# Performance work log

Hardware: AMD Instinct MI355X
Metric: run time of the kernel (lower is better)

## Reference

```python
import jax, jax.numpy as jnp
import numpy as np

SEQ_LEN = 12          # seq_length
K = 8                 # nsamples = 2 * num_samples
RADII = (4.0 + 1e-06, 8.0 + 1e-06, 12.0 + 1e-06)
COUT = (64, 128, 256)


def _group(xyz, s_xyz, radius):
    # ball query via knn + radius mask: xyz (B,N,3) queries, s_xyz (B,M,3) keys
    d2 = jnp.sum((xyz[:, :, None, :] - s_xyz[:, None, :, :]) ** 2, axis=-1)  # (B,N,M)
    neg, idx = jax.lax.top_k(-d2, K)                                          # (B,N,K)
    valid = (-neg) <= radius * radius
    # points outside the ball are replaced by the nearest neighbor (pad-with-first)
    return jnp.where(valid, idx, idx[..., :1])


def _gather(a, idx):
    # a (B,M,C), idx (B,N,K) -> (B,N,K,C)
    return jax.vmap(lambda t, i: t[i])(a, idx)


def _cell(xyz, feat, state, W, b, radius, cout):
    # PointRNN cell: group state points around current points, fuse
    # [displacement, current feature, state feature] with a shared linear,
    # then max-pool over the K neighbors. New state xyz = current xyz.
    B, N, _ = xyz.shape
    if state is None:
        s_xyz, s_feat = xyz, jnp.zeros((B, N, cout), xyz.dtype)
    else:
        s_xyz, s_feat = state
    idx = _group(xyz, s_xyz, radius)
    n_xyz = _gather(s_xyz, idx)                      # (B,N,K,3)
    n_feat = _gather(s_feat, idx)                    # (B,N,K,cout)
    disp = n_xyz - xyz[:, :, None, :]
    parts = [disp]
    if feat is not None:
        cin = feat.shape[-1]
        parts.append(jnp.broadcast_to(feat[:, :, None, :], (B, N, K, cin)))
    parts.append(n_feat)
    h = jnp.concatenate(parts, axis=-1) @ W + b      # (B,N,K,cout)
    return (xyz, jnp.max(h, axis=2))                 # (xyz, (B,N,cout))


def _forward(frames, W1, b1, W2, b2, W3, b3, Wm, bm, Wl, bl):
    half = SEQ_LEN // 2
    s1 = s2 = s3 = None
    # encode
    for i in range(half):
        s1 = _cell(frames[:, i], None, s1, W1, b1, RADII[0], COUT[0])
        s2 = _cell(s1[0], s1[1], s2, W2, b2, RADII[1], COUT[1])
        s3 = _cell(s2[0], s2[1], s3, W3, b3, RADII[2], COUT[2])
    # decode
    input_frame = frames[:, half - 1]
    preds = []
    for i in range(half, SEQ_LEN):
        s1 = _cell(input_frame, None, s1, W1, b1, RADII[0], COUT[0])
        s2 = _cell(s1[0], s1[1], s2, W2, b2, RADII[1], COUT[1])
        s3 = _cell(s2[0], s2[1], s3, W3, b3, RADII[2], COUT[2])
        h = jax.nn.relu(s3[1] @ Wm + bm)             # MLP([256,64]) = Lin+ReLU
        motion = h @ Wl + bl                         # (B,N,3)
        input_frame = input_frame + motion
        preds.append(input_frame)
    return jnp.stack(preds, axis=1)                  # (B, T/2, N, 3)


def setup_inputs() -> dict:
    key = jax.random.key(0)
    ks = jax.random.split(key, 12)
    B, N = 16, 512
    frames = jax.random.normal(ks[0], (B, SEQ_LEN, N, 3), jnp.float32) * 2.0

    def lin(k, fin, fout):
        k1, k2 = jax.random.split(k)
        s = 1.0 / np.sqrt(fin)
        return (jax.random.uniform(k1, (fin, fout), jnp.float32, -s, s),
                jax.random.uniform(k2, (fout,), jnp.float32, -s, s))

    W1, b1 = lin(ks[1], 3 + 0 + 64, 64)
    W2, b2 = lin(ks[2], 3 + 64 + 128, 128)
    W3, b3 = lin(ks[3], 3 + 128 + 256, 256)
    Wm, bm = lin(ks[4], 256, 64)
    Wl, bl = lin(ks[5], 64, 3)
    return {"frames": frames, "W1": W1, "b1": b1, "W2": W2, "b2": b2,
            "W3": W3, "b3": b3, "Wm": Wm, "bm": bm, "Wl": Wl, "bl": bl}


def reference(frames, W1, b1, W2, b2, W3, b3, Wm, bm, Wl, bl):
    return _forward(frames, W1, b1, W2, b2, W3, b3, Wm, bm, Wl, bl)
```

## Files before the change

### kernel.cpp

```cpp
#include <hip/hip_runtime.h>
#include <math.h>

#define BB 16
#define NN 512
#define KNN 8
#define SEQ 12
#define TQ 8
#define QB 32
#define PB 16

typedef __attribute__((ext_vector_type(8))) short bf8_t;
typedef __attribute__((ext_vector_type(4))) float f4_t;

__device__ __forceinline__ ushort f2b(float x) {
    uint u = __float_as_uint(x);
    return (ushort)((u + 0x7fffu + ((u >> 16) & 1u)) >> 16);
}
__device__ __forceinline__ float b2f(ushort h) {
    return __uint_as_float((uint)h << 16);
}
__device__ __forceinline__ void cvt8(const float* __restrict__ p,
                                     bf8_t& h, bf8_t& l) {
    float4 x0 = *(const float4*)p;
    float4 x1 = *(const float4*)(p + 4);
    float v[8] = {x0.x, x0.y, x0.z, x0.w, x1.x, x1.y, x1.z, x1.w};
#pragma unroll
    for (int i = 0; i < 8; ++i) {
        ushort hh = f2b(v[i]);
        h[i] = (short)hh;
        l[i] = (short)f2b(v[i] - b2f(hh));
    }
}

__global__ __launch_bounds__(256) void knn_kernel(
        const float* __restrict__ xq, int xq_bs,
        const float* __restrict__ xs, int xs_bs,
        int* __restrict__ idx1, int* __restrict__ idx2, int* __restrict__ idx3,
        float r2a, float r2b, float r2c, int warm) {
    __shared__ float s[NN * 3 + NN / 64];
    __shared__ float cd[QB][TQ][KNN + 1];
    __shared__ int   ci[QB][TQ][KNN + 1];
    int b = blockIdx.y;
    const float* xqp; const float* xsp; long iofs;
    if (warm) {
        int z = blockIdx.z;
        int qz = z < 5 ? z : 5;
        int sz = z - 1 < 0 ? 0 : z - 1;
        xqp = xq + (long)qz * NN * 3;
        xsp = xq + (long)sz * NN * 3;
        xs_bs = xq_bs;
        iofs = (long)z * BB * NN * KNN;
    } else {
        xqp = xq; xsp = xs; iofs = 0;
    }

    for (int j = threadIdx.x; j < NN; j += 256) {
        const float* p = xsp + (long)b * xs_bs + j * 3;
        int o = 3 * j + (j >> 6);
        s[o + 0] = p[0]; s[o + 1] = p[1]; s[o + 2] = p[2];
    }
    __syncthreads();

    int qi  = threadIdx.x / TQ;
    int sub = threadIdx.x % TQ;
    int n = blockIdx.x * QB + qi;
    const float* q = xqp + (long)b * xq_bs + n * 3;
    float qx = q[0], qy = q[1], qz2 = q[2];

    float bd[KNN];
    int   bi[KNN];
#pragma unroll
    for (int k = 0; k < KNN; ++k) { bd[k] = 1e30f; bi[k] = 0; }

    int j0 = sub * (NN / TQ);
    int sbase = 3 * j0 + sub;
#pragma unroll 4
    for (int jj = 0; jj < NN / TQ; ++jj) {
        float dx = s[sbase + 3 * jj + 0] - qx;
        float dy = s[sbase + 3 * jj + 1] - qy;
        float dz = s[sbase + 3 * jj + 2] - qz2;
        float d2 = fmaf(dx, dx, fmaf(dy, dy, dz * dz));
        if (d2 < bd[KNN - 1]) {
            bd[KNN - 1] = d2; bi[KNN - 1] = j0 + jj;
#pragma unroll
            for (int k = KNN - 1; k >= 1; --k) {
                if (bd[k] < bd[k - 1]) {
                    float td = bd[k]; bd[k] = bd[k - 1]; bd[k - 1] = td;
                    int   ti = bi[k]; bi[k] = bi[k - 1]; bi[k - 1] = ti;
                }
            }
        }
    }

#pragma unroll
    for (int k = 0; k < KNN; ++k) { cd[qi][sub][k] = bd[k]; ci[qi][sub][k] = bi[k]; }
    cd[qi][sub][KNN] = 1e30f; ci[qi][sub][KNN] = 0x7fffffff;
    __syncthreads();

    for (int stride = TQ / 2; stride >= 1; stride >>= 1) {
        if (sub < stride) {
            float rd[KNN]; int ri[KNN];
            int ia = 0, ib = 0;
#pragma unroll
            for (int k = 0; k < KNN; ++k) {
                float da = cd[qi][sub][ia], db = cd[qi][sub + stride][ib];
                int   ja = ci[qi][sub][ia], jb = ci[qi][sub + stride][ib];
                bool ta = (da < db) || (da == db && ja < jb);
                rd[k] = ta ? da : db; ri[k] = ta ? ja : jb;
                ia += ta ? 1 : 0; ib += ta ? 0 : 1;
            }
#pragma unroll
            for (int k = 0; k < KNN; ++k) { cd[qi][sub][k] = rd[k]; ci[qi][sub][k] = ri[k]; }
        }
        __syncthreads();
    }

    if (sub == 0) {
        long base = iofs + ((long)(b * NN + n)) * KNN;
        int i0 = ci[qi][0][0];
#pragma unroll
        for (int k = 0; k < KNN; ++k) {
            float d = cd[qi][0][k]; int j = ci[qi][0][k];
            idx1[base + k] = (d <= r2a) ? j : i0;
            idx2[base + k] = (d <= r2b) ? j : i0;
            idx3[base + k] = (d <= r2c) ? j : i0;
        }
    }
}

__global__ __launch_bounds__(256) void convW_kernel(
        const float* __restrict__ W1, const float* __restrict__ W2,
        const float* __restrict__ W3, const float* __restrict__ Wm,
        ushort* __restrict__ w1h, ushort* __restrict__ w1l,
        ushort* __restrict__ w2h, ushort* __restrict__ w2l,
        ushort* __restrict__ w3h, ushort* __restrict__ w3l,
        ushort* __restrict__ w2fh, ushort* __restrict__ w2fl,
        ushort* __restrict__ w3fh, ushort* __restrict__ w3fl,
        ushort* __restrict__ wmh, ushort* __restrict__ wml) {
    int t = blockIdx.x * 256 + threadIdx.x;
    float v; ushort* ph; ushort* pl; int idx;
    if (t < 4096)        { int n = t >> 6, k = t & 63;
        v = W1[(3 + k) * 64 + n];   ph = w1h;  pl = w1l;  idx = t; }
    else if (t < 20480)  { int u = t - 4096, n = u >> 7, k = u & 127;
        v = W2[(67 + k) * 128 + n]; ph = w2h;  pl = w2l;  idx = u; }
    else if (t < 86016)  { int u = t - 20480, n = u >> 8, k = u & 255;
        v = W3[(131 + k) * 256 + n]; ph = w3h; pl = w3l;  idx = u; }
    else if (t < 94208)  { int u = t - 86016, n = u >> 6, k = u & 63;
        v = W2[(3 + k) * 128 + n];  ph = w2fh; pl = w2fl; idx = u; }
    else if (t < 126976) { int u = t - 94208, n = u >> 7, k = u & 127;
        v = W3[(3 + k) * 256 + n];  ph = w3fh; pl = w3fl; idx = u; }
    else if (t < 143360) { int u = t - 126976, n = u >> 8, k = u & 255;
        v = Wm[k * 64 + n];         ph = wmh;  pl = wml;  idx = u; }
    else return;
    ushort h = f2b(v);
    ph[idx] = h; pl[idx] = f2b(v - b2f(h));
}

template<bool FIRST>
__global__ __launch_bounds__(512, 4) void cells_kernel(
        const float* __restrict__ xq, int xq_bs,
        const float* __restrict__ xs, int xs_bs,
        const int* __restrict__ i1, const int* __restrict__ i2,
        const int* __restrict__ i3,
        const float* __restrict__ G1p, const float* __restrict__ G2p,
        const float* __restrict__ G3p,
        ushort* __restrict__ s1h, ushort* __restrict__ s1l,
        ushort* __restrict__ s2h, ushort* __restrict__ s2l,
        ushort* __restrict__ s3h, ushort* __restrict__ s3l,
        const float* __restrict__ W1, const float* __restrict__ b1,
        const float* __restrict__ W2, const float* __restrict__ b2,
        const float* __restrict__ W3, const float* __restrict__ b3,
        const ushort* __restrict__ w2fh, const ushort* __restrict__ w2fl,
        const ushort* __restrict__ w3fh, const ushort* __restrict__ w3fl,
        const ushort* __restrict__ wmh, const ushort* __restrict__ wml,
        const float* __restrict__ bm,
        const float* __restrict__ Wl, const float* __restrict__ bl,
        float* __restrict__ xnext, int xn_bs, int do_head) {
    __shared__ float s1s[PB][68];
    __shared__ float s2s[PB][132];
    __shared__ float s3b[PB][260];
    __shared__ float hs[PB][64];
    __shared__ float dsp[3][PB][KNN][3];
    __shared__ int   jss[3][PB][KNN];

    const int tid = threadIdx.x;
    const int blk = blockIdx.x;
    const int xcd = blk & 7, slot = blk >> 3;
    const int b   = xcd * 2 + (slot >> 5);
    const int n0  = (slot & 31) << 4;
    const long row0 = (long)b * NN + n0;
    const long bN = (long)b * NN;
    const int wv = tid >> 6, lane = tid & 63;
    const int fm = lane & 15, quad = lane >> 4;

    for (int t = tid; t < 3 * PB * KNN; t += 512) {
        int r = t >> 7, rem = t & 127, p = rem >> 3, k = rem & 7;
        const int* ix = (r == 0) ? i1 : ((r == 1) ? i2 : i3);
        int j = ix[(row0 + p) * KNN + k];
        jss[r][p][k] = j;
        const float* sp = xs + (long)b * xs_bs + j * 3;
        const float* qp = xq + (long)b * xq_bs + (n0 + p) * 3;
        dsp[r][p][k][0] = sp[0] - qp[0];
        dsp[r][p][k][1] = sp[1] - qp[1];
        dsp[r][p][k][2] = sp[2] - qp[2];
    }
    __syncthreads();

    {
        int co = tid & 63, q = tid >> 6;
        float g1r[2][KNN];
        if (!FIRST) {
#pragma unroll
            for (int r = 0; r < 2; ++r)
#pragma unroll
                for (int k = 0; k < KNN; ++k)
                    g1r[r][k] = G1p[(bN + jss[0][2 * q + r][k]) * 64 + co];
        }
        float wx = W1[co], wy = W1[64 + co], wz = W1[128 + co];
        float bz = b1[co];
#pragma unroll
        for (int r = 0; r < 2; ++r) {
            int p = 2 * q + r;
            float acc = -1e30f;
#pragma unroll
            for (int k = 0; k < KNN; ++k) {
                float v = fmaf(dsp[0][p][k][0], wx, bz);
                v = fmaf(dsp[0][p][k][1], wy, v);
                v = fmaf(dsp[0][p][k][2], wz, v);
                if (!FIRST) v += g1r[r][k];
                acc = fmaxf(acc, v);
            }
            s1s[p][co] = acc;
            ushort h = f2b(acc);
            s1h[(row0 + p) * 64 + co] = h;
            s1l[(row0 + p) * 64 + co] = f2b(acc - b2f(h));
        }
    }
    __syncthreads();

    float4 g2r[KNN];
    {
        int c4 = tid & 31, g = tid >> 5;
        if (!FIRST) {
#pragma unroll
            for (int k = 0; k < KNN; ++k)
                g2r[k] = ((const float4*)G2p)[(bN + jss[1][g][k]) * 32 + c4];
        }
    }

    {
        int col = wv * 16 + fm;
        float bz = b2[col];
        f4_t acc = {bz, bz, bz, bz};
#pragma unroll
        for (int k0 = 0; k0 < 64; k0 += 32) {
            bf8_t ah, al; cvt8(&s1s[fm][k0 + quad * 8], ah, al);
            bf8_t bh = *(const bf8_t*)(w2fh + col * 64 + k0 + quad * 8);
            bf8_t bl = *(const bf8_t*)(w2fl + col * 64 + k0 + quad * 8);
            acc = __builtin_amdgcn_mfma_f32_16x16x32_bf16(ah, bh, acc, 0, 0, 0);
            acc = __builtin_amdgcn_mfma_f32_16x16x32_bf16(ah, bl, acc, 0, 0, 0);
            acc = __builtin_amdgcn_mfma_f32_16x16x32_bf16(al, bh, acc, 0, 0, 0);
        }
#pragma unroll
        for (int r = 0; r < 4; ++r) s2s[quad * 4 + r][col] = acc[r];
    }
    __syncthreads();

    {
        int c4 = tid & 31, g = tid >> 5;
        float4 bse = *(float4*)&s2s[g][c4 * 4];
        float4 wx = ((const float4*)W2)[c4];
        float4 wy = ((const float4*)(W2 + 128))[c4];
        float4 wz = ((const float4*)(W2 + 256))[c4];
        float4 m = make_float4(-1e30f, -1e30f, -1e30f, -1e30f);
#pragma unroll
        for (int k = 0; k < KNN; ++k) {
            float dx = dsp[1][g][k][0], dy = dsp[1][g][k][1], dz = dsp[1][g][k][2];
            float4 v;
            v.x = fmaf(dz, wz.x, fmaf(dy, wy.x, fmaf(dx, wx.x, bse.x)));
            v.y = fmaf(dz, wz.y, fmaf(dy, wy.y, fmaf(dx, wx.y, bse.y)));
            v.z = fmaf(dz, wz.z, fmaf(dy, wy.z, fmaf(dx, wx.z, bse.z)));
            v.w = fmaf(dz, wz.w, fmaf(dy, wy.w, fmaf(dx, wx.w, bse.w)));
            if (!FIRST) {
                v.x += g2r[k].x; v.y += g2r[k].y;
                v.z += g2r[k].z; v.w += g2r[k].w;
            }
            m.x = fmaxf(m.x, v.x); m.y = fmaxf(m.y, v.y);
            m.z = fmaxf(m.z, v.z); m.w = fmaxf(m.w, v.w);
        }
        *(float4*)&s2s[g][c4 * 4] = m;
        ushort4 mh, ml;
        mh.x = f2b(m.x); ml.x = f2b(m.x - b2f(mh.x));
        mh.y = f2b(m.y); ml.y = f2b(m.y - b2f(mh.y));
        mh.z = f2b(m.z); ml.z = f2b(m.z - b2f(mh.z));
        mh.w = f2b(m.w); ml.w = f2b(m.w - b2f(mh.w));
        *(ushort4*)&s2h[(row0 + g) * 128 + c4 * 4] = mh;
        *(ushort4*)&s2l[(row0 + g) * 128 + c4 * 4] = ml;
    }
    __syncthreads();

    float4 g3r[2][KNN];
    {
        int c4 = tid & 63, g = tid >> 6;
        if (!FIRST) {
#pragma unroll
            for (int r = 0; r < 2; ++r)
#pragma unroll
                for (int k = 0; k < KNN; ++k)
                    g3r[r][k] = ((const float4*)G3p)[(bN + jss[2][2 * g + r][k]) * 64 + c4];
        }
    }

    {
        int col0 = wv * 16 + fm, col1 = (wv + 8) * 16 + fm;
        float bz0 = b3[col0], bz1 = b3[col1];
        f4_t a0 = {bz0, bz0, bz0, bz0};
        f4_t a1 = {bz1, bz1, bz1, bz1};
#pragma unroll
        for (int k0 = 0; k0 < 128; k0 += 32) {
            bf8_t ah, al; cvt8(&s2s[fm][k0 + quad * 8], ah, al);
            bf8_t b0h = *(const bf8_t*)(w3fh + col0 * 128 + k0 + quad * 8);
            bf8_t b0l = *(const bf8_t*)(w3fl + col0 * 128 + k0 + quad * 8);
            bf8_t b1h = *(const bf8_t*)(w3fh + col1 * 128 + k0 + quad * 8);
            bf8_t b1l = *(const bf8_t*)(w3fl + col1 * 128 + k0 + quad * 8);
            a0 = __builtin_amdgcn_mfma_f32_16x16x32_bf16(ah, b0h, a0, 0, 0, 0);
            a0 = __builtin_amdgcn_mfma_f32_16x16x32_bf16(ah, b0l, a0, 0, 0, 0);
            a0 = __builtin_amdgcn_mfma_f32_16x16x32_bf16(al, b0h, a0, 0, 0, 0);
            a1 = __builtin_amdgcn_mfma_f32_16x16x32_bf16(ah, b1h, a1, 0, 0, 0);
            a1 = __builtin_amdgcn_mfma_f32_16x16x32_bf16(ah, b1l, a1, 0, 0, 0);
            a1 = __builtin_amdgcn_mfma_f32_16x16x32_bf16(al, b1h, a1, 0, 0, 0);
        }
#pragma unroll
        for (int r = 0; r < 4; ++r) {
            s3b[quad * 4 + r][col0] = a0[r];
            s3b[quad * 4 + r][col1] = a1[r];
        }
    }
    __syncthreads();

    {
        int c4 = tid & 63, g = tid >> 6;
        float4 wx = ((const float4*)W3)[c4];
        float4 wy = ((const float4*)(W3 + 256))[c4];
        float4 wz = ((const float4*)(W3 + 512))[c4];
#pragma unroll
        for (int r = 0; r < 2; ++r) {
            int p = 2 * g + r;
            float4 bse = *(float4*)&s3b[p][c4 * 4];
            float4 m = make_float4(-1e30f, -1e30f, -1e30f, -1e30f);
#pragma unroll
            for (int k = 0; k < KNN; ++k) {
                float dx = dsp[2][p][k][0], dy = dsp[2][p][k][1], dz = dsp[2][p][k][2];
                float4 v;
                v.x = fmaf(dz, wz.x, fmaf(dy, wy.x, fmaf(dx, wx.x, bse.x)));
                v.y = fmaf(dz, wz.y, fmaf(dy, wy.y, fmaf(dx, wx.y, bse.y)));
                v.z = fmaf(dz, wz.z, fmaf(dy, wy.z, fmaf(dx, wx.z, bse.z)));
                v.w = fmaf(dz, wz.w, fmaf(dy, wy.w, fmaf(dx, wx.w, bse.w)));
                if (!FIRST) {
                    v.x += g3r[r][k].x; v.y += g3r[r][k].y;
                    v.z += g3r[r][k].z; v.w += g3r[r][k].w;
                }
                m.x = fmaxf(m.x, v.x); m.y = fmaxf(m.y, v.y);
                m.z = fmaxf(m.z, v.z); m.w = fmaxf(m.w, v.w);
            }
            *(float4*)&s3b[p][c4 * 4] = m;
            ushort4 mh, ml;
            mh.x = f2b(m.x); ml.x = f2b(m.x - b2f(mh.x));
            mh.y = f2b(m.y); ml.y = f2b(m.y - b2f(mh.y));
            mh.z = f2b(m.z); ml.z = f2b(m.z - b2f(mh.z));
            mh.w = f2b(m.w); ml.w = f2b(m.w - b2f(mh.w));
            *(ushort4*)&s3h[(row0 + p) * 256 + c4 * 4] = mh;
            *(ushort4*)&s3l[(row0 + p) * 256 + c4 * 4] = ml;
        }
    }

    if (do_head) {
        __syncthreads();
        if (wv < 4) {
            int col = wv * 16 + fm;
            float bz = bm[col];
            f4_t acc = {bz, bz, bz, bz};
#pragma unroll
            for (int k0 = 0; k0 < 256; k0 += 32) {
                bf8_t ah, al; cvt8(&s3b[fm][k0 + quad * 8], ah, al);
                bf8_t bh = *(const bf8_t*)(wmh + col * 256 + k0 + quad * 8);
                bf8_t bl = *(const bf8_t*)(wml + col * 256 + k0 + quad * 8);
                acc = __builtin_amdgcn_mfma_f32_16x16x32_bf16(ah, bh, acc, 0, 0, 0);
                acc = __builtin_amdgcn_mfma_f32_16x16x32_bf16(ah, bl, acc, 0, 0, 0);
                acc = __builtin_amdgcn_mfma_f32_16x16x32_bf16(al, bh, acc, 0, 0, 0);
            }
#pragma unroll
            for (int r = 0; r < 4; ++r)
                hs[quad * 4 + r][col] = fmaxf(acc[r], 0.f);
        }
        __syncthreads();
        if (tid < PB * 3) {
            int p = tid / 3, d = tid % 3;
            float m = bl[d];
#pragma unroll 4
            for (int c = 0; c < 64; ++c)
                m = fmaf(hs[p][c], Wl[c * 3 + d], m);
            const float* qp = xq + (long)b * xq_bs + (n0 + p) * 3;
            xnext[(long)b * xn_bs + (n0 + p) * 3 + d] = qp[d] + m;
        }
    }
}

template<int N>
__device__ __forceinline__ void gemmTile(
        const ushort* __restrict__ Ah, const ushort* __restrict__ Al,
        const ushort* __restrict__ Bh, const ushort* __restrict__ Bl,
        float* __restrict__ G, int rb, int cb, int tid, ushort* lds) {
    const int row0 = rb * 128, c0 = cb * 64;
    ushort* ah = lds;
    ushort* al = lds + 128 * 40;
    ushort* bh = lds + 256 * 40;
    ushort* bl = lds + 320 * 40;
    const int wv = tid >> 6, lane = tid & 63;
    const int m = lane & 15, quad = lane >> 4;
    const int wm0 = wv * 32;
    const int lr = tid >> 2, ls = (tid & 3) * 8;

    f4_t acc[2][4];
#pragma unroll
    for (int rt = 0; rt < 2; ++rt)
#pragma unroll
        for (int ct = 0; ct < 4; ++ct) acc[rt][ct] = (f4_t){0.f, 0.f, 0.f, 0.f};

    bf8_t pah0, pah1, pal0, pal1, pbh, pbl;
    pah0 = *(const bf8_t*)(Ah + (long)(row0 + lr) * N + ls);
    pah1 = *(const bf8_t*)(Ah + (long)(row0 + 64 + lr) * N + ls);
    pal0 = *(const bf8_t*)(Al + (long)(row0 + lr) * N + ls);
    pal1 = *(const bf8_t*)(Al + (long)(row0 + 64 + lr) * N + ls);
    pbh  = *(const bf8_t*)(Bh + (long)(c0 + lr) * N + ls);
    pbl  = *(const bf8_t*)(Bl + (long)(c0 + lr) * N + ls);

    for (int k0 = 0; k0 < N; k0 += 32) {
        if (k0) __syncthreads();
        *(bf8_t*)(ah + lr * 40 + ls) = pah0;
        *(bf8_t*)(ah + (64 + lr) * 40 + ls) = pah1;
        *(bf8_t*)(al + lr * 40 + ls) = pal0;
        *(bf8_t*)(al + (64 + lr) * 40 + ls) = pal1;
        *(bf8_t*)(bh + lr * 40 + ls) = pbh;
        *(bf8_t*)(bl + lr * 40 + ls) = pbl;
        __syncthreads();
        if (k0 + 32 < N) {
            int kn = k0 + 32;
            pah0 = *(const bf8_t*)(Ah + (long)(row0 + lr) * N + kn + ls);
            pah1 = *(const bf8_t*)(Ah + (long)(row0 + 64 + lr) * N + kn + ls);
            pal0 = *(const bf8_t*)(Al + (long)(row0 + lr) * N + kn + ls);
            pal1 = *(const bf8_t*)(Al + (long)(row0 + 64 + lr) * N + kn + ls);
            pbh  = *(const bf8_t*)(Bh + (long)(c0 + lr) * N + kn + ls);
            pbl  = *(const bf8_t*)(Bl + (long)(c0 + lr) * N + kn + ls);
        }
        bf8_t a0h = *(const bf8_t*)(ah + (wm0 + m) * 40 + quad * 8);
        bf8_t a0l = *(const bf8_t*)(al + (wm0 + m) * 40 + quad * 8);
        bf8_t a1h = *(const bf8_t*)(ah + (wm0 + 16 + m) * 40 + quad * 8);
        bf8_t a1l = *(const bf8_t*)(al + (wm0 + 16 + m) * 40 + quad * 8);
#pragma unroll
        for (int ct = 0; ct < 4; ++ct) {
            bf8_t bth = *(const bf8_t*)(bh + (ct * 16 + m) * 40 + quad * 8);
            bf8_t btl = *(const bf8_t*)(bl + (ct * 16 + m) * 40 + quad * 8);
            acc[0][ct] = __builtin_amdgcn_mfma_f32_16x16x32_bf16(a0h, bth, acc[0][ct], 0, 0, 0);
            acc[0][ct] = __builtin_amdgcn_mfma_f32_16x16x32_bf16(a0h, btl, acc[0][ct], 0, 0, 0);
            acc[0][ct] = __builtin_amdgcn_mfma_f32_16x16x32_bf16(a0l, bth, acc[0][ct], 0, 0, 0);
            acc[1][ct] = __builtin_amdgcn_mfma_f32_16x16x32_bf16(a1h, bth, acc[1][ct], 0, 0, 0);
            acc[1][ct] = __builtin_amdgcn_mfma_f32_16x16x32_bf16(a1h, btl, acc[1][ct], 0, 0, 0);
            acc[1][ct] = __builtin_amdgcn_mfma_f32_16x16x32_bf16(a1l, bth, acc[1][ct], 0, 0, 0);
        }
    }
#pragma unroll
    for (int rt = 0; rt < 2; ++rt)
#pragma unroll
        for (int ct = 0; ct < 4; ++ct) {
            int col = c0 + ct * 16 + m;
#pragma unroll
            for (int r = 0; r < 4; ++r)
                G[(long)(row0 + wm0 + rt * 16 + quad * 4 + r) * N + col] = acc[rt][ct][r];
        }
}

__global__ __launch_bounds__(256) void gemmG_kernel(
        const ushort* __restrict__ s1h, const ushort* __restrict__ s1l,
        const ushort* __restrict__ s2h, const ushort* __restrict__ s2l,
        const ushort* __restrict__ s3h, const ushort* __restrict__ s3l,
        const ushort* __restrict__ w1h, const ushort* __restrict__ w1l,
        const ushort* __restrict__ w2h, const ushort* __restrict__ w2l,
        const ushort* __restrict__ w3h, const ushort* __restrict__ w3l,
        float* __restrict__ G1, float* __restrict__ G2,
        float* __restrict__ G3) {
    __shared__ ushort lds[384 * 40];
    int bx = blockIdx.x, tid = threadIdx.x;
    if (bx < 256) {
        int xcd = bx & 7, rem = bx >> 3;
        int rb = xcd * 8 + (rem & 7), cb = rem >> 3;
        gemmTile<256>(s3h, s3l, w3h, w3l, G3, rb, cb, tid, lds);
    } else if (bx < 384) {
        int u = bx - 256; int xcd = u & 7, rem = u >> 3;
        int rb = xcd * 8 + (rem & 7), cb = rem >> 3;
        gemmTile<128>(s2h, s2l, w2h, w2l, G2, rb, cb, tid, lds);
    } else {
        int u = bx - 384; int xcd = u & 7, j = u >> 3;
        gemmTile<64>(s1h, s1l, w1h, w1l, G1, xcd * 8 + j, 0, tid, lds);
    }
}

extern "C" void kernel_launch(void* const* d_in, const int* in_sizes, int n_in,
                              void* d_out, int out_size, void* d_ws, size_t ws_size,
                              hipStream_t stream) {
    const float* frames = (const float*)d_in[0];
    const float* W1 = (const float*)d_in[1]; const float* b1 = (const float*)d_in[2];
    const float* W2 = (const float*)d_in[3]; const float* b2 = (const float*)d_in[4];
    const float* W3 = (const float*)d_in[5]; const float* b3 = (const float*)d_in[6];
    const float* Wm = (const float*)d_in[7]; const float* bm = (const float*)d_in[8];
    const float* Wl = (const float*)d_in[9]; const float* bl = (const float*)d_in[10];
    float* out = (float*)d_out;

    const long M = (long)BB * NN;
    float* ws = (float*)d_ws;
    float* G1b = ws; ws += M * 64;
    float* G2b = ws; ws += M * 128;
    float* G3b = ws; ws += M * 256;
    ushort* us = (ushort*)ws;
    ushort* s1h = us; us += M * 64;   ushort* s1l = us; us += M * 64;
    ushort* s2h = us; us += M * 128;  ushort* s2l = us; us += M * 128;
    ushort* s3h = us; us += M * 256;  ushort* s3l = us; us += M * 256;
    ushort* w1h = us; us += 4096;     ushort* w1l = us; us += 4096;
    ushort* w2h = us; us += 16384;    ushort* w2l = us; us += 16384;
    ushort* w3h = us; us += 65536;    ushort* w3l = us; us += 65536;
    ushort* w2fh = us; us += 8192;    ushort* w2fl = us; us += 8192;
    ushort* w3fh = us; us += 32768;   ushort* w3fl = us; us += 32768;
    ushort* wmh = us; us += 16384;    ushort* wml = us; us += 16384;
    const long BNK = M * KNN;
    int* ip = (int*)us;
    int* idx1w = ip; ip += 7 * BNK;
    int* idx2w = ip; ip += 7 * BNK;
    int* idx3w = ip; ip += 7 * BNK;

    double ra = 4.0 + 1e-6, rb = 8.0 + 1e-6, rc = 12.0 + 1e-6;
    float r2a = (float)(ra * ra), r2b = (float)(rb * rb), r2c = (float)(rc * rc);

    const int FB = SEQ * NN * 3;
    const int OB = 6 * NN * 3;

    convW_kernel<<<560, 256, 0, stream>>>(W1, W2, W3, Wm,
                                          w1h, w1l, w2h, w2l, w3h, w3l,
                                          w2fh, w2fl, w3fh, w3fl, wmh, wml);
    knn_kernel<<<dim3(NN / QB, BB, 7), 256, 0, stream>>>(
        frames, FB, nullptr, 0, idx1w, idx2w, idx3w, r2a, r2b, r2c, 1);

    for (int t = 0; t < SEQ; ++t) {
        const float* xq; int xq_bs;
        const float* xs; int xs_bs;
        if (t < 6)       { xq = frames + (long)t * NN * 3;        xq_bs = FB; }
        else if (t == 6) { xq = frames + 5L * NN * 3;             xq_bs = FB; }
        else             { xq = out + (long)(t - 7) * NN * 3;     xq_bs = OB; }
        if (t == 0)      { xs = xq;                               xs_bs = xq_bs; }
        else if (t <= 6) { xs = frames + (long)(t - 1) * NN * 3;  xs_bs = FB; }
        else if (t == 7) { xs = frames + 5L * NN * 3;             xs_bs = FB; }
        else             { xs = out + (long)(t - 8) * NN * 3;     xs_bs = OB; }

        int slot = (t <= 6) ? t : 0;
        int* i1 = idx1w + slot * BNK;
        int* i2 = idx2w + slot * BNK;
        int* i3 = idx3w + slot * BNK;

        if (t >= 7)
            knn_kernel<<<dim3(NN / QB, BB, 1), 256, 0, stream>>>(
                xq, xq_bs, xs, xs_bs, i1, i2, i3, r2a, r2b, r2c, 0);

        int do_head = (t >= 6);
        float* xnext = do_head ? out + (long)(t - 6) * NN * 3 : nullptr;

        if (t == 0)
            cells_kernel<true><<<BB * NN / PB, 512, 0, stream>>>(
                xq, xq_bs, xs, xs_bs, i1, i2, i3,
                G1b, G2b, G3b, s1h, s1l, s2h, s2l, s3h, s3l,
                W1, b1, W2, b2, W3, b3,
                w2fh, w2fl, w3fh, w3fl, wmh, wml, bm,
                Wl, bl, xnext, OB, do_head);
        else
            cells_kernel<false><<<BB * NN / PB, 512, 0, stream>>>(
                xq, xq_bs, xs, xs_bs, i1, i2, i3,
                G1b, G2b, G3b, s1h, s1l, s2h, s2l, s3h, s3l,
                W1, b1, W2, b2, W3, b3,
                w2fh, w2fl, w3fh, w3fl, wmh, wml, bm,
                Wl, bl, xnext, OB, do_head);

        if (t < SEQ - 1)
            gemmG_kernel<<<448, 256, 0, stream>>>(
                s1h, s1l, s2h, s2l, s3h, s3l,
                w1h, w1l, w2h, w2l, w3h, w3l,
                G1b, G2b, G3b);
    }
}
```

Before: 555.6 us.

## Fuse decode KNN into gemmG launch and store bf16 hi/lo splits in LDS

Decode-step KNN for the next timestep is now computed by extra blocks appended to the G-matrix GEMM launch, removing a separate kernel launch and letting KNN overlap the GEMM. The cells kernel stores hi/lo bf16 splits of intermediate states directly in a pooled, aliased LDS buffer instead of fp32 arrays that were re-converted before each MFMA. This trades repeated conversion work for extra LDS stores and more careful shared-memory aliasing.

```diff
diff --git a/kernel.cpp b/kernel.cpp
--- a/kernel.cpp
+++ b/kernel.cpp
@@ -18,18 +18,6 @@
 }
 __device__ __forceinline__ float b2f(ushort h) {
     return __uint_as_float((uint)h << 16);
-}
-__device__ __forceinline__ void cvt8(const float* __restrict__ p,
-                                     bf8_t& h, bf8_t& l) {
-    float4 x0 = *(const float4*)p;
-    float4 x1 = *(const float4*)(p + 4);
-    float v[8] = {x0.x, x0.y, x0.z, x0.w, x1.x, x1.y, x1.z, x1.w};
-#pragma unroll
-    for (int i = 0; i < 8; ++i) {
-        ushort hh = f2b(v[i]);
-        h[i] = (short)hh;
-        l[i] = (short)f2b(v[i] - b2f(hh));
-    }
 }
 
 __global__ __launch_bounds__(256) void knn_kernel(
@@ -121,6 +109,91 @@
 #pragma unroll
         for (int k = 0; k < KNN; ++k) {
             float d = cd[qi][0][k]; int j = ci[qi][0][k];
+            idx1[base + k] = (d <= r2a) ? j : i0;
+            idx2[base + k] = (d <= r2b) ? j : i0;
+            idx3[base + k] = (d <= r2c) ? j : i0;
+        }
+    }
+}
+
+__device__ void knn_core(const float* __restrict__ xq, int xq_bs,
+                         const float* __restrict__ xs, int xs_bs,
+                         int* __restrict__ idx1, int* __restrict__ idx2,
+                         int* __restrict__ idx3,
+                         float r2a, float r2b, float r2c,
+                         int bx, int b, int tid, char* smem) {
+    float* s  = (float*)smem;
+    float* cd = s + 1544;
+    int*   ci = (int*)(cd + 2304);
+
+    for (int j = tid; j < NN; j += 256) {
+        const float* p = xs + (long)b * xs_bs + j * 3;
+        int o = 3 * j + (j >> 6);
+        s[o + 0] = p[0]; s[o + 1] = p[1]; s[o + 2] = p[2];
+    }
+    __syncthreads();
+
+    int qi = tid / TQ, sub = tid % TQ;
+    int n = bx * QB + qi;
+    const float* q = xq + (long)b * xq_bs + n * 3;
+    float qx = q[0], qy = q[1], qz2 = q[2];
+
+    float bd[KNN]; int bi[KNN];
+#pragma unroll
+    for (int k = 0; k < KNN; ++k) { bd[k] = 1e30f; bi[k] = 0; }
+
+    int j0 = sub * (NN / TQ);
+    int sbase = 3 * j0 + sub;
+#pragma unroll 4
+    for (int jj = 0; jj < NN / TQ; ++jj) {
+        float dx = s[sbase + 3 * jj + 0] - qx;
+        float dy = s[sbase + 3 * jj + 1] - qy;
+        float dz = s[sbase + 3 * jj + 2] - qz2;
+        float d2 = fmaf(dx, dx, fmaf(dy, dy, dz * dz));
+        if (d2 < bd[KNN - 1]) {
+            bd[KNN - 1] = d2; bi[KNN - 1] = j0 + jj;
+#pragma unroll
+            for (int k = KNN - 1; k >= 1; --k) {
+                if (bd[k] < bd[k - 1]) {
+                    float td = bd[k]; bd[k] = bd[k - 1]; bd[k - 1] = td;
+                    int   ti = bi[k]; bi[k] = bi[k - 1]; bi[k - 1] = ti;
+                }
+            }
+        }
+    }
+
+    int b9 = (qi * 8 + sub) * 9;
+#pragma unroll
+    for (int k = 0; k < KNN; ++k) { cd[b9 + k] = bd[k]; ci[b9 + k] = bi[k]; }
+    cd[b9 + KNN] = 1e30f; ci[b9 + KNN] = 0x7fffffff;
+    __syncthreads();
+
+    for (int stride = TQ / 2; stride >= 1; stride >>= 1) {
+        if (sub < stride) {
+            int a9 = (qi * 8 + sub) * 9, c9 = (qi * 8 + sub + stride) * 9;
+            float rd[KNN]; int ri[KNN];
+            int ia = 0, ib = 0;
+#pragma unroll
+            for (int k = 0; k < KNN; ++k) {
+                float da = cd[a9 + ia], db = cd[c9 + ib];
+                int   ja = ci[a9 + ia], jb = ci[c9 + ib];
+                bool ta = (da < db) || (da == db && ja < jb);
+                rd[k] = ta ? da : db; ri[k] = ta ? ja : jb;
+                ia += ta ? 1 : 0; ib += ta ? 0 : 1;
+            }
+#pragma unroll
+            for (int k = 0; k < KNN; ++k) { cd[a9 + k] = rd[k]; ci[a9 + k] = ri[k]; }
+        }
+        __syncthreads();
+    }
+
+    if (sub == 0) {
+        int a9 = (qi * 8) * 9;
+        long base = ((long)(b * NN + n)) * KNN;
+        int i0 = ci[a9];
+#pragma unroll
+        for (int k = 0; k < KNN; ++k) {
+            float d = cd[a9 + k]; int j = ci[a9 + k];
             idx1[base + k] = (d <= r2a) ? j : i0;
             idx2[base + k] = (d <= r2b) ? j : i0;
             idx3[base + k] = (d <= r2c) ? j : i0;
@@ -176,12 +249,18 @@
         const float* __restrict__ bm,
         const float* __restrict__ Wl, const float* __restrict__ bl,
         float* __restrict__ xnext, int xn_bs, int do_head) {
-    __shared__ float s1s[PB][68];
-    __shared__ float s2s[PB][132];
-    __shared__ float s3b[PB][260];
-    __shared__ float hs[PB][64];
-    __shared__ float dsp[3][PB][KNN][3];
-    __shared__ int   jss[3][PB][KNN];
+    __shared__ __attribute__((aligned(16))) char pool[44544];
+    float*  dspf = (float*)pool;
+    int*    jssp = (int*)(pool + 4608);
+    ushort* s1H  = (ushort*)(pool + 6144);
+    ushort* s1L  = (ushort*)(pool + 8448);
+    float*  s2sp = (float*)(pool + 10752);
+    ushort* s2H  = (ushort*)(pool + 19200);
+    ushort* s2L  = (ushort*)(pool + 23552);
+    float*  s3bp = (float*)(pool + 27904);
+    ushort* s3H  = (ushort*)(pool + 6144);
+    ushort* s3L  = (ushort*)(pool + 14592);
+    float*  hsp  = (float*)pool;
 
     const int tid = threadIdx.x;
     const int blk = blockIdx.x;
@@ -197,12 +276,12 @@
         int r = t >> 7, rem = t & 127, p = rem >> 3, k = rem & 7;
         const int* ix = (r == 0) ? i1 : ((r == 1) ? i2 : i3);
         int j = ix[(row0 + p) * KNN + k];
-        jss[r][p][k] = j;
+        jssp[t] = j;
         const float* sp = xs + (long)b * xs_bs + j * 3;
         const float* qp = xq + (long)b * xq_bs + (n0 + p) * 3;
-        dsp[r][p][k][0] = sp[0] - qp[0];
-        dsp[r][p][k][1] = sp[1] - qp[1];
-        dsp[r][p][k][2] = sp[2] - qp[2];
+        dspf[t * 3 + 0] = sp[0] - qp[0];
+        dspf[t * 3 + 1] = sp[1] - qp[1];
+        dspf[t * 3 + 2] = sp[2] - qp[2];
     }
     __syncthreads();
 
@@ -214,7 +293,7 @@
             for (int r = 0; r < 2; ++r)
 #pragma unroll
                 for (int k = 0; k < KNN; ++k)
-                    g1r[r][k] = G1p[(bN + jss[0][2 * q + r][k]) * 64 + co];
+                    g1r[r][k] = G1p[(bN + jssp[(2 * q + r) * 8 + k]) * 64 + co];
         }
         float wx = W1[co], wy = W1[64 + co], wz = W1[128 + co];
         float bz = b1[co];
@@ -224,16 +303,19 @@
             float acc = -1e30f;
 #pragma unroll
             for (int k = 0; k < KNN; ++k) {
-                float v = fmaf(dsp[0][p][k][0], wx, bz);
-                v = fmaf(dsp[0][p][k][1], wy, v);
-                v = fmaf(dsp[0][p][k][2], wz, v);
+                int di = (p * 8 + k) * 3;
+                float v = fmaf(dspf[di + 0], wx, bz);
+                v = fmaf(dspf[di + 1], wy, v);
+                v = fmaf(dspf[di + 2], wz, v);
                 if (!FIRST) v += g1r[r][k];
                 acc = fmaxf(acc, v);
             }
-            s1s[p][co] = acc;
             ushort h = f2b(acc);
+            ushort l = f2b(acc - b2f(h));
             s1h[(row0 + p) * 64 + co] = h;
-            s1l[(row0 + p) * 64 + co] = f2b(acc - b2f(h));
+            s1l[(row0 + p) * 64 + co] = l;
+            s1H[p * 72 + co] = h;
+            s1L[p * 72 + co] = l;
         }
     }
     __syncthreads();
@@ -244,7 +326,7 @@
         if (!FIRST) {
 #pragma unroll
             for (int k = 0; k < KNN; ++k)
-                g2r[k] = ((const float4*)G2p)[(bN + jss[1][g][k]) * 32 + c4];
+                g2r[k] = ((const float4*)G2p)[(bN + jssp[(16 + g) * 8 + k]) * 32 + c4];
         }
     }
 
@@ -254,7 +336,8 @@
         f4_t acc = {bz, bz, bz, bz};
 #pragma unroll
         for (int k0 = 0; k0 < 64; k0 += 32) {
-            bf8_t ah, al; cvt8(&s1s[fm][k0 + quad * 8], ah, al);
+            bf8_t ah = *(const bf8_t*)(s1H + fm * 72 + k0 + quad * 8);
+            bf8_t al = *(const bf8_t*)(s1L + fm * 72 + k0 + quad * 8);
             bf8_t bh = *(const bf8_t*)(w2fh + col * 64 + k0 + quad * 8);
             bf8_t bl = *(const bf8_t*)(w2fl + col * 64 + k0 + quad * 8);
             acc = __builtin_amdgcn_mfma_f32_16x16x32_bf16(ah, bh, acc, 0, 0, 0);
@@ -262,20 +345,21 @@
             acc = __builtin_amdgcn_mfma_f32_16x16x32_bf16(al, bh, acc, 0, 0, 0);
         }
 #pragma unroll
-        for (int r = 0; r < 4; ++r) s2s[quad * 4 + r][col] = acc[r];
+        for (int r = 0; r < 4; ++r) s2sp[(quad * 4 + r) * 132 + col] = acc[r];
     }
     __syncthreads();
 
     {
         int c4 = tid & 31, g = tid >> 5;
-        float4 bse = *(float4*)&s2s[g][c4 * 4];
+        float4 bse = *(float4*)&s2sp[g * 132 + c4 * 4];
         float4 wx = ((const float4*)W2)[c4];
         float4 wy = ((const float4*)(W2 + 128))[c4];
         float4 wz = ((const float4*)(W2 + 256))[c4];
         float4 m = make_float4(-1e30f, -1e30f, -1e30f, -1e30f);
 #pragma unroll
         for (int k = 0; k < KNN; ++k) {
-            float dx = dsp[1][g][k][0], dy = dsp[1][g][k][1], dz = dsp[1][g][k][2];
+            int di = ((16 + g) * 8 + k) * 3;
+            float dx = dspf[di + 0], dy = dspf[di + 1], dz = dspf[di + 2];
             float4 v;
             v.x = fmaf(dz, wz.x, fmaf(dy, wy.x, fmaf(dx, wx.x, bse.x)));
             v.y = fmaf(dz, wz.y, fmaf(dy, wy.y, fmaf(dx, wx.y, bse.y)));
@@ -288,7 +372,6 @@
             m.x = fmaxf(m.x, v.x); m.y = fmaxf(m.y, v.y);
             m.z = fmaxf(m.z, v.z); m.w = fmaxf(m.w, v.w);
         }
-        *(float4*)&s2s[g][c4 * 4] = m;
         ushort4 mh, ml;
         mh.x = f2b(m.x); ml.x = f2b(m.x - b2f(mh.x));
         mh.y = f2b(m.y); ml.y = f2b(m.y - b2f(mh.y));
@@ -296,6 +379,8 @@
         mh.w = f2b(m.w); ml.w = f2b(m.w - b2f(mh.w));
         *(ushort4*)&s2h[(row0 + g) * 128 + c4 * 4] = mh;
         *(ushort4*)&s2l[(row0 + g) * 128 + c4 * 4] = ml;
+        *(ushort4*)(s2H + g * 136 + c4 * 4) = mh;
+        *(ushort4*)(s2L + g * 136 + c4 * 4) = ml;
     }
     __syncthreads();
 
@@ -307,7 +392,7 @@
             for (int r = 0; r < 2; ++r)
 #pragma unroll
                 for (int k = 0; k < KNN; ++k)
-                    g3r[r][k] = ((const float4*)G3p)[(bN + jss[2][2 * g + r][k]) * 64 + c4];
+                    g3r[r][k] = ((const float4*)G3p)[(bN + jssp[(32 + 2 * g + r) * 8 + k]) * 64 + c4];
         }
     }
 
@@ -318,7 +403,8 @@
         f4_t a1 = {bz1, bz1, bz1, bz1};
 #pragma unroll
         for (int k0 = 0; k0 < 128; k0 += 32) {
-            bf8_t ah, al; cvt8(&s2s[fm][k0 + quad * 8], ah, al);
+            bf8_t ah = *(const bf8_t*)(s2H + fm * 136 + k0 + quad * 8);
+            bf8_t al = *(const bf8_t*)(s2L + fm * 136 + k0 + quad * 8);
             bf8_t b0h = *(const bf8_t*)(w3fh + col0 * 128 + k0 + quad * 8);
             bf8_t b0l = *(const bf8_t*)(w3fl + col0 * 128 + k0 + quad * 8);
             bf8_t b1h = *(const bf8_t*)(w3fh + col1 * 128 + k0 + quad * 8);
@@ -332,8 +418,8 @@
         }
 #pragma unroll
         for (int r = 0; r < 4; ++r) {
-            s3b[quad * 4 + r][col0] = a0[r];
-            s3b[quad * 4 + r][col1] = a1[r];
+            s3bp[(quad * 4 + r) * 260 + col0] = a0[r];
+            s3bp[(quad * 4 + r) * 260 + col1] = a1[r];
         }
     }
     __syncthreads();
@@ -346,11 +432,12 @@
 #pragma unroll
         for (int r = 0; r < 2; ++r) {
             int p = 2 * g + r;
-            float4 bse = *(float4*)&s3b[p][c4 * 4];
+            float4 bse = *(float4*)&s3bp[p * 260 + c4 * 4];
             float4 m = make_float4(-1e30f, -1e30f, -1e30f, -1e30f);
 #pragma unroll
             for (int k = 0; k < KNN; ++k) {
-                float dx = dsp[2][p][k][0], dy = dsp[2][p][k][1], dz = dsp[2][p][k][2];
+                int di = ((32 + p) * 8 + k) * 3;
+                float dx = dspf[di + 0], dy = dspf[di + 1], dz = dspf[di + 2];
                 float4 v;
                 v.x = fmaf(dz, wz.x, fmaf(dy, wy.x, fmaf(dx, wx.x, bse.x)));
                 v.y = fmaf(dz, wz.y, fmaf(dy, wy.y, fmaf(dx, wx.y, bse.y)));
@@ -363,7 +450,6 @@
                 m.x = fmaxf(m.x, v.x); m.y = fmaxf(m.y, v.y);
                 m.z = fmaxf(m.z, v.z); m.w = fmaxf(m.w, v.w);
             }
-            *(float4*)&s3b[p][c4 * 4] = m;
             ushort4 mh, ml;
             mh.x = f2b(m.x); ml.x = f2b(m.x - b2f(mh.x));
             mh.y = f2b(m.y); ml.y = f2b(m.y - b2f(mh.y));
@@ -371,6 +457,10 @@
             mh.w = f2b(m.w); ml.w = f2b(m.w - b2f(mh.w));
             *(ushort4*)&s3h[(row0 + p) * 256 + c4 * 4] = mh;
             *(ushort4*)&s3l[(row0 + p) * 256 + c4 * 4] = ml;
+            if (do_head) {
+                *(ushort4*)(s3H + p * 264 + c4 * 4) = mh;
+                *(ushort4*)(s3L + p * 264 + c4 * 4) = ml;
+            }
         }
     }
 
@@ -382,7 +472,8 @@
             f4_t acc = {bz, bz, bz, bz};
 #pragma unroll
             for (int k0 = 0; k0 < 256; k0 += 32) {
-                bf8_t ah, al; cvt8(&s3b[fm][k0 + quad * 8], ah, al);
+                bf8_t ah = *(const bf8_t*)(s3H + fm * 264 + k0 + quad * 8);
+                bf8_t al = *(const bf8_t*)(s3L + fm * 264 + k0 + quad * 8);
                 bf8_t bh = *(const bf8_t*)(wmh + col * 256 + k0 + quad * 8);
                 bf8_t bl = *(const bf8_t*)(wml + col * 256 + k0 + quad * 8);
                 acc = __builtin_amdgcn_mfma_f32_16x16x32_bf16(ah, bh, acc, 0, 0, 0);
@@ -391,7 +482,7 @@
             }
 #pragma unroll
             for (int r = 0; r < 4; ++r)
-                hs[quad * 4 + r][col] = fmaxf(acc[r], 0.f);
+                hsp[(quad * 4 + r) * 64 + col] = fmaxf(acc[r], 0.f);
         }
         __syncthreads();
         if (tid < PB * 3) {
@@ -399,7 +490,7 @@
             float m = bl[d];
 #pragma unroll 4
             for (int c = 0; c < 64; ++c)
-                m = fmaf(hs[p][c], Wl[c * 3 + d], m);
+                m = fmaf(hsp[p * 64 + c], Wl[c * 3 + d], m);
             const float* qp = xq + (long)b * xq_bs + (n0 + p) * 3;
             xnext[(long)b * xn_bs + (n0 + p) * 3 + d] = qp[d] + m;
         }
@@ -480,7 +571,7 @@
         }
 }
 
-__global__ __launch_bounds__(256) void gemmG_kernel(
+__global__ __launch_bounds__(256) void gemmG_knn_kernel(
         const ushort* __restrict__ s1h, const ushort* __restrict__ s1l,
         const ushort* __restrict__ s2h, const ushort* __restrict__ s2l,
         const ushort* __restrict__ s3h, const ushort* __restrict__ s3l,
@@ -488,20 +579,28 @@
         const ushort* __restrict__ w2h, const ushort* __restrict__ w2l,
         const ushort* __restrict__ w3h, const ushort* __restrict__ w3l,
         float* __restrict__ G1, float* __restrict__ G2,
-        float* __restrict__ G3) {
-    __shared__ ushort lds[384 * 40];
+        float* __restrict__ G3,
+        const float* __restrict__ kxq, int kxq_bs,
+        const float* __restrict__ kxs, int kxs_bs,
+        int* __restrict__ ki1, int* __restrict__ ki2, int* __restrict__ ki3,
+        float r2a, float r2b, float r2c) {
+    __shared__ __attribute__((aligned(16))) char smem[30720];
     int bx = blockIdx.x, tid = threadIdx.x;
     if (bx < 256) {
         int xcd = bx & 7, rem = bx >> 3;
         int rb = xcd * 8 + (rem & 7), cb = rem >> 3;
-        gemmTile<256>(s3h, s3l, w3h, w3l, G3, rb, cb, tid, lds);
+        gemmTile<256>(s3h, s3l, w3h, w3l, G3, rb, cb, tid, (ushort*)smem);
     } else if (bx < 384) {
         int u = bx - 256; int xcd = u & 7, rem = u >> 3;
         int rb = xcd * 8 + (rem & 7), cb = rem >> 3;
-        gemmTile<128>(s2h, s2l, w2h, w2l, G2, rb, cb, tid, lds);
+        gemmTile<128>(s2h, s2l, w2h, w2l, G2, rb, cb, tid, (ushort*)smem);
+    } else if (bx < 448) {
+        int u = bx - 384; int xcd = u & 7, j = u >> 3;
+        gemmTile<64>(s1h, s1l, w1h, w1l, G1, xcd * 8 + j, 0, tid, (ushort*)smem);
     } else {
-        int u = bx - 384; int xcd = u & 7, j = u >> 3;
-        gemmTile<64>(s1h, s1l, w1h, w1l, G1, xcd * 8 + j, 0, tid, lds);
+        int u = bx - 448;
+        knn_core(kxq, kxq_bs, kxs, kxs_bs, ki1, ki2, ki3,
+                 r2a, r2b, r2c, u & 15, u >> 4, tid, smem);
     }
 }
 
@@ -565,10 +664,6 @@
         int* i2 = idx2w + slot * BNK;
         int* i3 = idx3w + slot * BNK;
 
-        if (t >= 7)
-            knn_kernel<<<dim3(NN / QB, BB, 1), 256, 0, stream>>>(
-                xq, xq_bs, xs, xs_bs, i1, i2, i3, r2a, r2b, r2c, 0);
-
         int do_head = (t >= 6);
         float* xnext = do_head ? out + (long)(t - 6) * NN * 3 : nullptr;
 
@@ -587,10 +682,21 @@
                 w2fh, w2fl, w3fh, w3fl, wmh, wml, bm,
                 Wl, bl, xnext, OB, do_head);
 
-        if (t < SEQ - 1)
-            gemmG_kernel<<<448, 256, 0, stream>>>(
+        if (t < SEQ - 1) {
+            bool dk = (t + 1 >= 7);
+            const float* kxq = frames; int kxq_bs = FB;
+            const float* kxs = frames; int kxs_bs = FB;
+            if (dk) {
+                kxq = out + (long)(t + 1 - 7) * NN * 3; kxq_bs = OB;
+                if (t + 1 == 7) { kxs = frames + 5L * NN * 3; kxs_bs = FB; }
+                else            { kxs = out + (long)(t + 1 - 8) * NN * 3; kxs_bs = OB; }
+            }
+            gemmG_knn_kernel<<<448 + (dk ? 256 : 0), 256, 0, stream>>>(
                 s1h, s1l, s2h, s2l, s3h, s3l,
                 w1h, w1l, w2h, w2l, w3h, w3l,
-                G1b, G2b, G3b);
-    }
-}
+                G1b, G2b, G3b,
+                kxq, kxq_bs, kxs, kxs_bs,
+                idx1w, idx2w, idx3w, r2a, r2b, r2c);
+        }
+    }
+}
```

Result: slower. 594.4 us (+7.0%).

## Pack cell LDS into aliased pool, stage bf16 splits, skip last-step state writes

Applied to the files above, without the earlier changes.

The separate shared arrays become one aliased byte pool, which cuts the LDS footprint per block and may let more blocks stay resident. Intermediate s1 and s2 states are kept in LDS as bf16 hi/lo pairs, so the MFMA operands are read directly and the per-load cvt8 split is no longer needed. On the final timestep, global writes of the bf16 state are skipped because no later gemmG consumes them. Aliasing buffers across phases risks read-after-write hazards if the barrier placement does not cover every reuse.

```diff
diff --git a/kernel.cpp b/kernel.cpp
--- a/kernel.cpp
+++ b/kernel.cpp
@@ -175,13 +175,17 @@
         const ushort* __restrict__ wmh, const ushort* __restrict__ wml,
         const float* __restrict__ bm,
         const float* __restrict__ Wl, const float* __restrict__ bl,
-        float* __restrict__ xnext, int xn_bs, int do_head) {
-    __shared__ float s1s[PB][68];
-    __shared__ float s2s[PB][132];
-    __shared__ float s3b[PB][260];
-    __shared__ float hs[PB][64];
-    __shared__ float dsp[3][PB][KNN][3];
-    __shared__ int   jss[3][PB][KNN];
+        float* __restrict__ xnext, int xn_bs, int do_head, int do_g) {
+    __shared__ __attribute__((aligned(16))) char pool[31488];
+    float*  dspf = (float*)pool;
+    int*    jssp = (int*)(pool + 4608);
+    ushort* s2H  = (ushort*)(pool + 6144);
+    ushort* s2L  = (ushort*)(pool + 10496);
+    ushort* s1H  = (ushort*)(pool + 14848);
+    ushort* s1L  = (ushort*)(pool + 17152);
+    float*  s2sp = (float*)(pool + 19456);
+    float*  s3bp = (float*)(pool + 14848);
+    float*  hsp  = (float*)pool;
 
     const int tid = threadIdx.x;
     const int blk = blockIdx.x;
@@ -197,12 +201,12 @@
         int r = t >> 7, rem = t & 127, p = rem >> 3, k = rem & 7;
         const int* ix = (r == 0) ? i1 : ((r == 1) ? i2 : i3);
         int j = ix[(row0 + p) * KNN + k];
-        jss[r][p][k] = j;
+        jssp[t] = j;
         const float* sp = xs + (long)b * xs_bs + j * 3;
         const float* qp = xq + (long)b * xq_bs + (n0 + p) * 3;
-        dsp[r][p][k][0] = sp[0] - qp[0];
-        dsp[r][p][k][1] = sp[1] - qp[1];
-        dsp[r][p][k][2] = sp[2] - qp[2];
+        dspf[t * 3 + 0] = sp[0] - qp[0];
+        dspf[t * 3 + 1] = sp[1] - qp[1];
+        dspf[t * 3 + 2] = sp[2] - qp[2];
     }
     __syncthreads();
 
@@ -214,7 +218,7 @@
             for (int r = 0; r < 2; ++r)
 #pragma unroll
                 for (int k = 0; k < KNN; ++k)
-                    g1r[r][k] = G1p[(bN + jss[0][2 * q + r][k]) * 64 + co];
+                    g1r[r][k] = G1p[(bN + jssp[(2 * q + r) * 8 + k]) * 64 + co];
         }
         float wx = W1[co], wy = W1[64 + co], wz = W1[128 + co];
         float bz = b1[co];
@@ -224,16 +228,21 @@
             float acc = -1e30f;
 #pragma unroll
             for (int k = 0; k < KNN; ++k) {
-                float v = fmaf(dsp[0][p][k][0], wx, bz);
-                v = fmaf(dsp[0][p][k][1], wy, v);
-                v = fmaf(dsp[0][p][k][2], wz, v);
+                int di = (p * 8 + k) * 3;
+                float v = fmaf(dspf[di + 0], wx, bz);
+                v = fmaf(dspf[di + 1], wy, v);
+                v = fmaf(dspf[di + 2], wz, v);
                 if (!FIRST) v += g1r[r][k];
                 acc = fmaxf(acc, v);
             }
-            s1s[p][co] = acc;
             ushort h = f2b(acc);
-            s1h[(row0 + p) * 64 + co] = h;
-            s1l[(row0 + p) * 64 + co] = f2b(acc - b2f(h));
+            ushort l = f2b(acc - b2f(h));
+            if (do_g) {
+                s1h[(row0 + p) * 64 + co] = h;
+                s1l[(row0 + p) * 64 + co] = l;
+            }
+            s1H[p * 72 + co] = h;
+            s1L[p * 72 + co] = l;
         }
     }
     __syncthreads();
@@ -244,7 +253,7 @@
         if (!FIRST) {
 #pragma unroll
             for (int k = 0; k < KNN; ++k)
-                g2r[k] = ((const float4*)G2p)[(bN + jss[1][g][k]) * 32 + c4];
+                g2r[k] = ((const float4*)G2p)[(bN + jssp[(16 + g) * 8 + k]) * 32 + c4];
         }
     }
 
@@ -254,7 +263,8 @@
         f4_t acc = {bz, bz, bz, bz};
 #pragma unroll
         for (int k0 = 0; k0 < 64; k0 += 32) {
-            bf8_t ah, al; cvt8(&s1s[fm][k0 + quad * 8], ah, al);
+            bf8_t ah = *(const bf8_t*)(s1H + fm * 72 + k0 + quad * 8);
+            bf8_t al = *(const bf8_t*)(s1L + fm * 72 + k0 + quad * 8);
             bf8_t bh = *(const bf8_t*)(w2fh + col * 64 + k0 + quad * 8);
             bf8_t bl = *(const bf8_t*)(w2fl + col * 64 + k0 + quad * 8);
             acc = __builtin_amdgcn_mfma_f32_16x16x32_bf16(ah, bh, acc, 0, 0, 0);
@@ -262,20 +272,21 @@
             acc = __builtin_amdgcn_mfma_f32_16x16x32_bf16(al, bh, acc, 0, 0, 0);
         }
 #pragma unroll
-        for (int r = 0; r < 4; ++r) s2s[quad * 4 + r][col] = acc[r];
+        for (int r = 0; r < 4; ++r) s2sp[(quad * 4 + r) * 132 + col] = acc[r];
     }
     __syncthreads();
 
     {
         int c4 = tid & 31, g = tid >> 5;
-        float4 bse = *(float4*)&s2s[g][c4 * 4];
+        float4 bse = *(float4*)&s2sp[g * 132 + c4 * 4];
         float4 wx = ((const float4*)W2)[c4];
         float4 wy = ((const float4*)(W2 + 128))[c4];
         float4 wz = ((const float4*)(W2 + 256))[c4];
         float4 m = make_float4(-1e30f, -1e30f, -1e30f, -1e30f);
 #pragma unroll
         for (int k = 0; k < KNN; ++k) {
-            float dx = dsp[1][g][k][0], dy = dsp[1][g][k][1], dz = dsp[1][g][k][2];
+            int di = ((16 + g) * 8 + k) * 3;
+            float dx = dspf[di + 0], dy = dspf[di + 1], dz = dspf[di + 2];
             float4 v;
             v.x = fmaf(dz, wz.x, fmaf(dy, wy.x, fmaf(dx, wx.x, bse.x)));
             v.y = fmaf(dz, wz.y, fmaf(dy, wy.y, fmaf(dx, wx.y, bse.y)));
@@ -288,14 +299,17 @@
             m.x = fmaxf(m.x, v.x); m.y = fmaxf(m.y, v.y);
             m.z = fmaxf(m.z, v.z); m.w = fmaxf(m.w, v.w);
         }
-        *(float4*)&s2s[g][c4 * 4] = m;
         ushort4 mh, ml;
         mh.x = f2b(m.x); ml.x = f2b(m.x - b2f(mh.x));
         mh.y = f2b(m.y); ml.y = f2b(m.y - b2f(mh.y));
         mh.z = f2b(m.z); ml.z = f2b(m.z - b2f(mh.z));
         mh.w = f2b(m.w); ml.w = f2b(m.w - b2f(mh.w));
-        *(ushort4*)&s2h[(row0 + g) * 128 + c4 * 4] = mh;
-        *(ushort4*)&s2l[(row0 + g) * 128 + c4 * 4] = ml;
+        if (do_g) {
+            *(ushort4*)&s2h[(row0 + g) * 128 + c4 * 4] = mh;
+            *(ushort4*)&s2l[(row0 + g) * 128 + c4 * 4] = ml;
+        }
+        *(ushort4*)(s2H + g * 136 + c4 * 4) = mh;
+        *(ushort4*)(s2L + g * 136 + c4 * 4) = ml;
     }
     __syncthreads();
 
@@ -307,7 +321,7 @@
             for (int r = 0; r < 2; ++r)
 #pragma unroll
                 for (int k = 0; k < KNN; ++k)
-                    g3r[r][k] = ((const float4*)G3p)[(bN + jss[2][2 * g + r][k]) * 64 + c4];
+                    g3r[r][k] = ((const float4*)G3p)[(bN + jssp[(32 + 2 * g + r) * 8 + k]) * 64 + c4];
         }
     }
 
@@ -318,7 +332,8 @@
         f4_t a1 = {bz1, bz1, bz1, bz1};
 #pragma unroll
         for (int k0 = 0; k0 < 128; k0 += 32) {
-            bf8_t ah, al; cvt8(&s2s[fm][k0 + quad * 8], ah, al);
+            bf8_t ah = *(const bf8_t*)(s2H + fm * 136 + k0 + quad * 8);
+            bf8_t al = *(const bf8_t*)(s2L + fm * 136 + k0 + quad * 8);
             bf8_t b0h = *(const bf8_t*)(w3fh + col0 * 128 + k0 + quad * 8);
             bf8_t b0l = *(const bf8_t*)(w3fl + col0 * 128 + k0 + quad * 8);
             bf8_t b1h = *(const bf8_t*)(w3fh + col1 * 128 + k0 + quad * 8);
@@ -332,8 +347,8 @@
         }
 #pragma unroll
         for (int r = 0; r < 4; ++r) {
-            s3b[quad * 4 + r][col0] = a0[r];
-            s3b[quad * 4 + r][col1] = a1[r];
+            s3bp[(quad * 4 + r) * 260 + col0] = a0[r];
+            s3bp[(quad * 4 + r) * 260 + col1] = a1[r];
         }
     }
     __syncthreads();
@@ -346,11 +361,12 @@
 #pragma unroll
         for (int r = 0; r < 2; ++r) {
             int p = 2 * g + r;
-            float4 bse = *(float4*)&s3b[p][c4 * 4];
+            float4 bse = *(float4*)&s3bp[p * 260 + c4 * 4];
             float4 m = make_float4(-1e30f, -1e30f, -1e30f, -1e30f);
 #pragma unroll
             for (int k = 0; k < KNN; ++k) {
-                float dx = dsp[2][p][k][0], dy = dsp[2][p][k][1], dz = dsp[2][p][k][2];
+                int di = ((32 + p) * 8 + k) * 3;
+                float dx = dspf[di + 0], dy = dspf[di + 1], dz = dspf[di + 2];
                 float4 v;
                 v.x = fmaf(dz, wz.x, fmaf(dy, wy.x, fmaf(dx, wx.x, bse.x)));
                 v.y = fmaf(dz, wz.y, fmaf(dy, wy.y, fmaf(dx, wx.y, bse.y)));
@@ -363,14 +379,16 @@
                 m.x = fmaxf(m.x, v.x); m.y = fmaxf(m.y, v.y);
                 m.z = fmaxf(m.z, v.z); m.w = fmaxf(m.w, v.w);
             }
-            *(float4*)&s3b[p][c4 * 4] = m;
-            ushort4 mh, ml;
-            mh.x = f2b(m.x); ml.x = f2b(m.x - b2f(mh.x));
-            mh.y = f2b(m.y); ml.y = f2b(m.y - b2f(mh.y));
-            mh.z = f2b(m.z); ml.z = f2b(m.z - b2f(mh.z));
-            mh.w = f2b(m.w); ml.w = f2b(m.w - b2f(mh.w));
-            *(ushort4*)&s3h[(row0 + p) * 256 + c4 * 4] = mh;
-            *(ushort4*)&s3l[(row0 + p) * 256 + c4 * 4] = ml;
+            *(float4*)&s3bp[p * 260 + c4 * 4] = m;
+            if (do_g) {
+                ushort4 mh, ml;
+                mh.x = f2b(m.x); ml.x = f2b(m.x - b2f(mh.x));
+                mh.y = f2b(m.y); ml.y = f2b(m.y - b2f(mh.y));
+                mh.z = f2b(m.z); ml.z = f2b(m.z - b2f(mh.z));
+                mh.w = f2b(m.w); ml.w = f2b(m.w - b2f(mh.w));
+                *(ushort4*)&s3h[(row0 + p) * 256 + c4 * 4] = mh;
+                *(ushort4*)&s3l[(row0 + p) * 256 + c4 * 4] = ml;
+            }
         }
     }
 
@@ -382,7 +400,7 @@
             f4_t acc = {bz, bz, bz, bz};
 #pragma unroll
             for (int k0 = 0; k0 < 256; k0 += 32) {
-                bf8_t ah, al; cvt8(&s3b[fm][k0 + quad * 8], ah, al);
+                bf8_t ah, al; cvt8(&s3bp[fm * 260 + k0 + quad * 8], ah, al);
                 bf8_t bh = *(const bf8_t*)(wmh + col * 256 + k0 + quad * 8);
                 bf8_t bl = *(const bf8_t*)(wml + col * 256 + k0 + quad * 8);
                 acc = __builtin_amdgcn_mfma_f32_16x16x32_bf16(ah, bh, acc, 0, 0, 0);
@@ -391,7 +409,7 @@
             }
 #pragma unroll
             for (int r = 0; r < 4; ++r)
-                hs[quad * 4 + r][col] = fmaxf(acc[r], 0.f);
+                hsp[(quad * 4 + r) * 64 + col] = fmaxf(acc[r], 0.f);
         }
         __syncthreads();
         if (tid < PB * 3) {
@@ -399,7 +417,7 @@
             float m = bl[d];
 #pragma unroll 4
             for (int c = 0; c < 64; ++c)
-                m = fmaf(hs[p][c], Wl[c * 3 + d], m);
+                m = fmaf(hsp[p * 64 + c], Wl[c * 3 + d], m);
             const float* qp = xq + (long)b * xq_bs + (n0 + p) * 3;
             xnext[(long)b * xn_bs + (n0 + p) * 3 + d] = qp[d] + m;
         }
@@ -570,6 +588,7 @@
                 xq, xq_bs, xs, xs_bs, i1, i2, i3, r2a, r2b, r2c, 0);
 
         int do_head = (t >= 6);
+        int do_g = (t < SEQ - 1);
         float* xnext = do_head ? out + (long)(t - 6) * NN * 3 : nullptr;
 
         if (t == 0)
@@ -578,14 +597,14 @@
                 G1b, G2b, G3b, s1h, s1l, s2h, s2l, s3h, s3l,
                 W1, b1, W2, b2, W3, b3,
                 w2fh, w2fl, w3fh, w3fl, wmh, wml, bm,
-                Wl, bl, xnext, OB, do_head);
+                Wl, bl, xnext, OB, do_head, do_g);
         else
             cells_kernel<false><<<BB * NN / PB, 512, 0, stream>>>(
                 xq, xq_bs, xs, xs_bs, i1, i2, i3,
                 G1b, G2b, G3b, s1h, s1l, s2h, s2l, s3h, s3l,
                 W1, b1, W2, b2, W3, b3,
                 w2fh, w2fl, w3fh, w3fl, wmh, wml, bm,
-                Wl, bl, xnext, OB, do_head);
+                Wl, bl, xnext, OB, do_head, do_g);
 
         if (t < SEQ - 1)
             gemmG_kernel<<<448, 256, 0, stream>>>(
```

After: 559.8 us. No clear change (+0.7%).
